# Kernel optimization log

Measured on AMD Instinct MI355X. Metric: run time of the kernel, lower is better.

## Reference

```python
import jax, jax.numpy as jnp
import numpy as np

# pywt coif5 dec_lo (30 taps)
COIF5_DEC_LO = np.array([
    -9.517657273819165e-08, -1.6744288576823017e-07, 2.0637618513646814e-06,
    3.7346551751414047e-06, -2.1315026809955787e-05, -4.134043227251251e-05,
    0.00014054114970203437, 0.00030225958181306315, -0.0006381313430451114,
    -0.0016628637020130838, 0.0024333732126576722, 0.006764185448053083,
    -0.009164231162481846, -0.01976177894257264, 0.03268357426711183,
    0.0412892087501817, -0.10557420870333893, -0.06203596396290357,
    0.4379916261718371, 0.7742896036529562, 0.4215662066908515,
    -0.05204316317624377, -0.09192001055969624, 0.02816802897093635,
    0.023408156785839195, -0.010131117519849788, -0.004159358781386048,
    0.0021782363581090178, 0.00035858968789573785, -0.00021208083980379827,
], dtype=np.float32)


def _hilbert(x):
    # scipy.fftpack.hilbert: y_j = 1j*sign(j)*X_j, DC and Nyquist zeroed
    n = x.size
    X = np.fft.fft(x)
    sign = np.zeros(n)
    sign[1:(n + 1) // 2] = 1.0
    sign[n // 2 + 1:] = -1.0
    return np.real(np.fft.ifft(X * 1j * sign)).astype(np.float32)


def _make_filters():
    gl = COIF5_DEC_LO
    L = gl.size
    # QMF: dec_hi[k] = (-1)^(k+1) * dec_lo[L-1-k]
    gh = (((-1.0) ** (np.arange(L) + 1)) * gl[::-1]).astype(np.float32)
    fl = _hilbert(gl)
    fh = _hilbert(gh)
    return (jnp.asarray(gl), jnp.asarray(gh), jnp.asarray(fl), jnp.asarray(fh))


# torch bicubic (a=-0.75), scale 0.5, align_corners=False: src = 2*i + 0.5,
# fractional offset is always 0.5 -> fixed 4-tap stride-2 stencil.
_W0, _W1, _W2, _W3 = -0.09375, 0.59375, 0.59375, -0.09375


def _down2_last(x):
    # downsample last axis by 2 with edge-clamped borders (matches torch clamp)
    n = x.shape[-1]
    pad = [(0, 0)] * (x.ndim - 1) + [(1, 1)]
    xp = jnp.pad(x, pad, mode='edge')
    base = 2 * jnp.arange(n // 2)  # tap positions in padded coords
    return (_W0 * xp[..., base] + _W1 * xp[..., base + 1]
            + _W2 * xp[..., base + 2] + _W3 * xp[..., base + 3])


def _downsample(x):
    x = _down2_last(x)                                        # W axis
    x = jnp.swapaxes(_down2_last(jnp.swapaxes(x, -1, -2)), -1, -2)  # H axis
    return x


def _qwt(image, gl, gh, fl, fh):
    # In the source, _column/_row_convolve never shift X per tap and the
    # centered crop exactly removes the reflect padding, so
    # colfilter(X, h) == rowfilter(X, h) == X * sum(h)  (exact).
    filt = lambda x, h: x * jnp.sum(h)

    gl_d = _downsample(filt(image, gl))
    gh_d = _downsample(filt(image, gh))
    fl_d = _downsample(filt(image, fl))
    fh_d = _downsample(filt(image, fh))

    lglg = filt(gl_d, gl); lghg = filt(gl_d, gh); lglf = filt(gl_d, fl); lghf = filt(gl_d, fh)
    hglg = filt(gh_d, gl); hghg = filt(gh_d, gh); hglf = filt(gh_d, fl); hghf = filt(gh_d, fh)
    lflg = filt(fl_d, gl); lfhg = filt(fl_d, gh); lflf = filt(fl_d, fl); lfhf = filt(fl_d, fh)
    hflg = filt(fh_d, gl); hfhg = filt(fh_d, gh); hflf = filt(fh_d, fl); hfhf = filt(fh_d, fh)

    return (jnp.concatenate((lglg, lflg, lglf, lflf), axis=1),
            jnp.concatenate((lghg, lfhg, lghf, lfhf), axis=1),
            jnp.concatenate((hglg, hflg, hglf, hflf), axis=1),
            jnp.concatenate((hghg, hfhg, hghf, hfhf), axis=1))


def setup_inputs() -> dict:
    key = jax.random.key(0)
    image = jax.random.normal(key, (16, 3, 512, 512), dtype=jnp.float32)
    gl, gh, fl, fh = _make_filters()
    return {"image": image, "gl": gl, "gh": gh, "fl": fl, "fh": fh}


def reference(image, gl, gh, fl, fh):
    return _qwt(image, gl, gh, fl, fh)
```

## Files before the change

### kernel.cpp

```cpp
#include <hip/hip_runtime.h>


#define BW0 -0.09375f
#define BW1  0.59375f
#define BW2  0.59375f
#define BW3 -0.09375f

#define H_IN  512
#define W_IN  512
#define H_OUT 256
#define W_OUT 256
#define PLANE_OUT (H_OUT * W_OUT)
#define TENSOR_STRIDE (16 * 12 * PLANE_OUT)

__global__ __launch_bounds__(256) void qwt_fused_kernel(
    const float* __restrict__ img,
    const float* __restrict__ gl, const float* __restrict__ gh,
    const float* __restrict__ fl, const float* __restrict__ fh,
    float* __restrict__ out)
{
    __shared__ float s_scale[16];

    const int tid = threadIdx.x;

    if (tid < 64) {
        float vgl = 0.f, vgh = 0.f, vfl = 0.f, vfh = 0.f;
        if (tid < 30) { vgl = gl[tid]; vgh = gh[tid]; vfl = fl[tid]; vfh = fh[tid]; }
        #pragma unroll
        for (int m = 32; m >= 1; m >>= 1) {
            vgl += __shfl_xor(vgl, m);
            vgh += __shfl_xor(vgh, m);
            vfl += __shfl_xor(vfl, m);
            vfh += __shfl_xor(vfh, m);
        }
        if (tid < 16) {
            const int t = tid >> 2, cb = tid & 3;
            const float A = (t < 2) ? ((cb & 1) ? vfl : vgl)
                                    : ((cb & 1) ? vfh : vgh);
            const float B = (t & 1) ? ((cb < 2) ? vgh : vfh)
                                    : ((cb < 2) ? vgl : vfl);
            s_scale[tid] = A * B;
        }
    }
    __syncthreads();

    const int idx = blockIdx.x * 256 + tid;
    const int w4 = idx & 63;
    const int h  = (idx >> 6) & 255;
    const int bc = idx >> 14;
    const int c  = bc % 3;
    const int b  = bc / 3;

    const float* plane = img + (size_t)bc * (H_IN * W_IN);

    int r[4];
    #pragma unroll
    for (int i = 0; i < 4; ++i) {
        int rr = 2 * h - 1 + i;
        r[i] = rr < 0 ? 0 : (rr > H_IN - 1 ? H_IN - 1 : rr);
    }

    const int cbase = w4 * 8;
    int clo = cbase - 1; if (clo < 0) clo = 0;
    int chi = cbase + 8; if (chi > W_IN - 1) chi = W_IN - 1;

    float hv[4][4];
    #pragma unroll
    for (int i = 0; i < 4; ++i) {
        const float* rowp = plane + (size_t)r[i] * W_IN;
        const float4 a  = *(const float4*)(rowp + cbase);
        const float4 b4 = *(const float4*)(rowp + cbase + 4);
        const float v0 = rowp[clo];
        const float v9 = rowp[chi];
        const float v1 = a.x,  v2 = a.y,  v3 = a.z,  v4 = a.w;
        const float v5 = b4.x, v6 = b4.y, v7 = b4.z, v8 = b4.w;
        hv[i][0] = BW0 * v0 + BW1 * v1 + BW2 * v2 + BW3 * v3;
        hv[i][1] = BW0 * v2 + BW1 * v3 + BW2 * v4 + BW3 * v5;
        hv[i][2] = BW0 * v4 + BW1 * v5 + BW2 * v6 + BW3 * v7;
        hv[i][3] = BW0 * v6 + BW1 * v7 + BW2 * v8 + BW3 * v9;
    }

    float d[4];
    #pragma unroll
    for (int j = 0; j < 4; ++j)
        d[j] = BW0 * hv[0][j] + BW1 * hv[1][j] + BW2 * hv[2][j] + BW3 * hv[3][j];

    const size_t obase = (size_t)b * (12 * PLANE_OUT)
                       + (size_t)c * PLANE_OUT
                       + (size_t)h * W_OUT
                       + (size_t)(w4 * 4);
    #pragma unroll
    for (int t = 0; t < 4; ++t) {
        #pragma unroll
        for (int cb = 0; cb < 4; ++cb) {
            const float s = s_scale[t * 4 + cb];
            float4 o;
            o.x = d[0] * s; o.y = d[1] * s; o.z = d[2] * s; o.w = d[3] * s;
            *(float4*)(out + (size_t)t * TENSOR_STRIDE
                           + obase
                           + (size_t)cb * (3 * PLANE_OUT)) = o;
        }
    }
}

extern "C" void kernel_launch(void* const* d_in, const int* in_sizes, int n_in,
                              void* d_out, int out_size, void* d_ws, size_t ws_size,
                              hipStream_t stream) {
    const float* img = (const float*)d_in[0];
    const float* gl  = (const float*)d_in[1];
    const float* gh  = (const float*)d_in[2];
    const float* fl  = (const float*)d_in[3];
    const float* fh  = (const float*)d_in[4];
    float* out = (float*)d_out;

    const int threads = 256;
    const int blocks  = (16 * 3 * 256 * 256 / 4) / threads;
    qwt_fused_kernel<<<blocks, threads, 0, stream>>>(img, gl, gh, fl, fh, out);
}
```

Before: 241.4 us.

## Use shuffles for halo, nontemporal stores, and rotated store order

Replaces the two scalar halo loads per row with wavefront shuffles, since each wave covers a full 512-wide row (64 threads x 8 columns), and clamps the edges explicitly. Output stores become nontemporal vector stores so the large write stream skips cache retention. The 16 output planes are written in an order rotated per wave, which spreads concurrent writes across different memory regions. The rotation makes the store addresses depend on a runtime index, which costs extra address arithmetic.

```diff
diff --git a/kernel.cpp b/kernel.cpp
--- a/kernel.cpp
+++ b/kernel.cpp
@@ -12,6 +12,8 @@
 #define W_OUT 256
 #define PLANE_OUT (H_OUT * W_OUT)
 #define TENSOR_STRIDE (16 * 12 * PLANE_OUT)
+
+typedef float f4 __attribute__((ext_vector_type(4)));
 
 __global__ __launch_bounds__(256) void qwt_fused_kernel(
     const float* __restrict__ img,
@@ -61,8 +63,6 @@
     }
 
     const int cbase = w4 * 8;
-    int clo = cbase - 1; if (clo < 0) clo = 0;
-    int chi = cbase + 8; if (chi > W_IN - 1) chi = W_IN - 1;
 
     float hv[4][4];
     #pragma unroll
@@ -70,36 +70,38 @@
         const float* rowp = plane + (size_t)r[i] * W_IN;
         const float4 a  = *(const float4*)(rowp + cbase);
         const float4 b4 = *(const float4*)(rowp + cbase + 4);
-        const float v0 = rowp[clo];
-        const float v9 = rowp[chi];
         const float v1 = a.x,  v2 = a.y,  v3 = a.z,  v4 = a.w;
         const float v5 = b4.x, v6 = b4.y, v7 = b4.z, v8 = b4.w;
+        float v0 = __shfl_up(v8, 1);
+        float v9 = __shfl_down(v1, 1);
+        if (w4 == 0)  v0 = v1;
+        if (w4 == 63) v9 = v8;
         hv[i][0] = BW0 * v0 + BW1 * v1 + BW2 * v2 + BW3 * v3;
         hv[i][1] = BW0 * v2 + BW1 * v3 + BW2 * v4 + BW3 * v5;
         hv[i][2] = BW0 * v4 + BW1 * v5 + BW2 * v6 + BW3 * v7;
         hv[i][3] = BW0 * v6 + BW1 * v7 + BW2 * v8 + BW3 * v9;
     }
 
-    float d[4];
-    #pragma unroll
-    for (int j = 0; j < 4; ++j)
-        d[j] = BW0 * hv[0][j] + BW1 * hv[1][j] + BW2 * hv[2][j] + BW3 * hv[3][j];
+    float d0 = BW0 * hv[0][0] + BW1 * hv[1][0] + BW2 * hv[2][0] + BW3 * hv[3][0];
+    float d1 = BW0 * hv[0][1] + BW1 * hv[1][1] + BW2 * hv[2][1] + BW3 * hv[3][1];
+    float d2 = BW0 * hv[0][2] + BW1 * hv[1][2] + BW2 * hv[2][2] + BW3 * hv[3][2];
+    float d3 = BW0 * hv[0][3] + BW1 * hv[1][3] + BW2 * hv[2][3] + BW3 * hv[3][3];
 
     const size_t obase = (size_t)b * (12 * PLANE_OUT)
                        + (size_t)c * PLANE_OUT
                        + (size_t)h * W_OUT
                        + (size_t)(w4 * 4);
+    const int rot = (blockIdx.x + (tid >> 6)) & 15;
     #pragma unroll
-    for (int t = 0; t < 4; ++t) {
-        #pragma unroll
-        for (int cb = 0; cb < 4; ++cb) {
-            const float s = s_scale[t * 4 + cb];
-            float4 o;
-            o.x = d[0] * s; o.y = d[1] * s; o.z = d[2] * s; o.w = d[3] * s;
-            *(float4*)(out + (size_t)t * TENSOR_STRIDE
-                           + obase
-                           + (size_t)cb * (3 * PLANE_OUT)) = o;
-        }
+    for (int kk = 0; kk < 16; ++kk) {
+        const int k = (kk + rot) & 15;
+        const float s = s_scale[k];
+        f4 o;
+        o.x = d0 * s; o.y = d1 * s; o.z = d2 * s; o.w = d3 * s;
+        float* p = out + (size_t)(k >> 2) * TENSOR_STRIDE
+                       + obase
+                       + (size_t)(k & 3) * (3 * PLANE_OUT);
+        __builtin_nontemporal_store(o, (f4*)p);
     }
 }
 
```

New measurement: 243.6 us. About the same (+0.9%).
